# Performance work log

Measured on AMD Instinct MI355X. Metric: run time of the kernel, lower is better.

## Reference

```python
import jax, jax.numpy as jnp
import numpy as np

NUM_HEAD = 16

def _make_rope(max_len, dim_head, theta=10000.0):
    inv_freq = 1.0 / (theta ** (np.arange(0, dim_head, 2, dtype=np.float32) / dim_head))
    t = np.arange(max_len, dtype=np.float32)
    freqs = np.outer(t, inv_freq)  # [S, dim_head/2]
    return jnp.asarray(np.cos(freqs)), jnp.asarray(np.sin(freqs))

def setup_inputs() -> dict:
    key = jax.random.key(0)
    k1, k2, k3 = jax.random.split(key, 3)
    B, S, D = 2, 2048, 1024
    num_layer = 12
    std = 0.02 / np.sqrt(2 * num_layer)
    x = jax.random.normal(k1, (B, S, D), dtype=jnp.float32)
    wQKV = jax.random.normal(k2, (3 * D, D), dtype=jnp.float32) * std
    wOut = jax.random.normal(k3, (D, D), dtype=jnp.float32) * 0.02
    cos, sin = _make_rope(S, D // NUM_HEAD)
    return {"x": x, "wQKV": wQKV, "wOut": wOut, "cos": cos, "sin": sin}

def _apply_rope(t, cos, sin):
    # t: [B, H, S, dh]; cos/sin: [S, dh/2] -> broadcast [1,1,S,dh/2]
    te, to = t[..., ::2], t[..., 1::2]
    re = te * cos - to * sin
    ro = to * cos + te * sin
    return jnp.stack([re, ro], axis=-1).reshape(t.shape)

def reference(x, wQKV, wOut, cos, sin):
    B, S, D = x.shape
    H = NUM_HEAD
    dh = D // H
    qkv = x @ wQKV.T  # [B, S, 3D]
    q, k, v = jnp.split(qkv, 3, axis=-1)
    q = q.reshape(B, S, H, dh).transpose(0, 2, 1, 3)  # [B,H,S,dh]
    k = k.reshape(B, S, H, dh).transpose(0, 2, 1, 3)
    v = v.reshape(B, S, H, dh).transpose(0, 2, 1, 3)
    c = cos[:S][None, None]
    s = sin[:S][None, None]
    q = _apply_rope(q, c, s)
    k = _apply_rope(k, c, s)
    scores = jnp.einsum('bhsd,bhtd->bhst', q, k) / jnp.sqrt(jnp.asarray(dh, x.dtype))
    causal = jnp.tril(jnp.ones((S, S), dtype=bool))
    scores = jnp.where(causal, scores, jnp.asarray(-jnp.inf, scores.dtype))
    w = jax.nn.softmax(scores, axis=-1)
    out = jnp.einsum('bhst,bhtd->bhsd', w, v)  # [B,H,S,dh]
    out = out.transpose(0, 2, 1, 3).reshape(B, S, D)
    return out @ wOut.T
```

## Files before the change

kernel.cpp:

```cpp
#include <hip/hip_runtime.h>
#include <hip/hip_bf16.h>

typedef __attribute__((ext_vector_type(8))) short bf16x8;
typedef __attribute__((ext_vector_type(4))) short s16x4;
typedef __attribute__((ext_vector_type(4))) float f32x4;

__device__ __forceinline__ short f2bf(float f) {
    unsigned int u = __builtin_bit_cast(unsigned int, f);
    u += 0x7fffu + ((u >> 16) & 1u);
    return (short)(u >> 16);
}

#define GLDS(g, l) __builtin_amdgcn_global_load_lds( \
    (__attribute__((address_space(1))) void*)(g),    \
    (__attribute__((address_space(3))) void*)(l), 16, 0, 0)

#define BARSB() { __builtin_amdgcn_s_barrier(); __builtin_amdgcn_sched_barrier(0); }
#define VMC8()  { asm volatile("s_waitcnt vmcnt(8)" ::: "memory"); __builtin_amdgcn_sched_barrier(0); }
#define VMC7()  { asm volatile("s_waitcnt vmcnt(7)" ::: "memory"); __builtin_amdgcn_sched_barrier(0); }
#define VMC0()  { asm volatile("s_waitcnt vmcnt(0)" ::: "memory"); __builtin_amdgcn_sched_barrier(0); }

__global__ __launch_bounds__(256) void cvt_kernel(const float* __restrict__ in,
                                                  short* __restrict__ out, int n4) {
    int i = blockIdx.x * 256 + threadIdx.x;
    if (i >= n4) return;
    float4 v = reinterpret_cast<const float4*>(in)[i];
    s16x4 r = { f2bf(v.x), f2bf(v.y), f2bf(v.z), f2bf(v.w) };
    reinterpret_cast<s16x4*>(out)[i] = r;
}

#define LDP 72

__device__ __forceinline__ void load_a(const short* __restrict__ A, int wr, int lo, int hi,
                                       int mh, bf16x8 aF[4][2]) {
#pragma unroll
    for (int mi = 0; mi < 4; ++mi)
#pragma unroll
        for (int kk = 0; kk < 2; ++kk)
            aF[mi][kk] = *reinterpret_cast<const bf16x8*>(
                &A[(wr * 128 + mh * 64 + mi * 16 + lo) * 64 + (((kk * 4 + hi) ^ (lo & 7)) << 3)]);
}
__device__ __forceinline__ void load_b3(const short* __restrict__ B, int wc, int lo, int hi,
                                        bf16x8 bF[3][2]) {
#pragma unroll
    for (int ni = 0; ni < 3; ++ni)
#pragma unroll
        for (int kk = 0; kk < 2; ++kk)
            bF[ni][kk] = *reinterpret_cast<const bf16x8*>(
                &B[(wc * 48 + ni * 16 + lo) * 64 + (((kk * 4 + hi) ^ (lo & 7)) << 3)]);
}
__device__ __forceinline__ void mfma24(const bf16x8 aF[4][2], const bf16x8 bF[3][2],
                                       f32x4 acc[8][3], int mh) {
#pragma unroll
    for (int mi = 0; mi < 4; ++mi)
#pragma unroll
        for (int ni = 0; ni < 3; ++ni)
#pragma unroll
            for (int kk = 0; kk < 2; ++kk)
                acc[mh * 4 + mi][ni] = __builtin_amdgcn_mfma_f32_16x16x32_bf16(
                    aF[mi][kk], bF[ni][kk], acc[mh * 4 + mi][ni], 0, 0, 0);
}

__global__ __launch_bounds__(512, 1) void gemm_qkv_rope(
    const short* __restrict__ X, const short* __restrict__ W,
    const float* __restrict__ cosT, const float* __restrict__ sinT,
    short* __restrict__ Qo, short* __restrict__ Ko, short* __restrict__ Vo) {
    __shared__ short ldsA[2][16384];
    __shared__ short ldsB[2][12288];
    const int tid = threadIdx.x;
    const int lane = tid & 63;
    const int w = tid >> 6;
    const int lo = lane & 15, hi = lane >> 4;
    const int wr = w >> 2, wc = w & 3;
    const int lin = blockIdx.x;
    const int xcd = lin & 7;
    const int i_ = lin >> 3;
    const int m0 = ((xcd >> 1) * 4 + (i_ & 3)) * 256;
    const int n0 = ((xcd & 1) * 8 + (i_ >> 2)) * 192;

    f32x4 acc[8][3];
#pragma unroll
    for (int i = 0; i < 8; i++)
#pragma unroll
        for (int j = 0; j < 3; j++) acc[i][j] = {0.f, 0.f, 0.f, 0.f};

    const int srow8 = w * 8 + (lane >> 3);
    const int scx = (((lane & 7) ^ ((lane >> 3) & 7)) << 3);

#define STAGE_A(BUF, KT, IT) GLDS(X + (size_t)(m0 + (IT) * 64 + srow8) * 1024 + ((KT) << 6) + scx, \
                                  (char*)&ldsA[BUF][0] + (IT) * 8192 + w * 1024)
#define STAGE_B(BUF, KT, IT) GLDS(W + (size_t)(n0 + (IT) * 64 + srow8) * 1024 + ((KT) << 6) + scx, \
                                  (char*)&ldsB[BUF][0] + (IT) * 8192 + w * 1024)

    bf16x8 aF[4][2], bF[3][2];

    STAGE_B(0, 0, 0); STAGE_B(0, 0, 1); STAGE_B(0, 0, 2);
    STAGE_A(0, 0, 0); STAGE_A(0, 0, 1); STAGE_A(0, 0, 2); STAGE_A(0, 0, 3);

    for (int t = 0; t < 16; ++t) {
        const int c = t & 1;
        if (t < 15) {
            const int nb_ = c ^ 1, t1 = t + 1;
            STAGE_B(nb_, t1, 0); STAGE_B(nb_, t1, 1); STAGE_B(nb_, t1, 2);
            STAGE_A(nb_, t1, 0); STAGE_A(nb_, t1, 1); STAGE_A(nb_, t1, 2); STAGE_A(nb_, t1, 3);
            VMC7();
        } else {
            VMC0();
        }
        BARSB();
        load_a(&ldsA[c][0], wr, lo, hi, 0, aF);
        load_b3(&ldsB[c][0], wc, lo, hi, bF);
        mfma24(aF, bF, acc, 0);
        load_a(&ldsA[c][0], wr, lo, hi, 1, aF);
        mfma24(aF, bF, acc, 1);
        if (t < 15) BARSB();
    }
#undef STAGE_A
#undef STAGE_B

#pragma unroll
    for (int mi = 0; mi < 8; mi++) {
#pragma unroll
        for (int r = 0; r < 4; r++) {
            const int m = m0 + wr * 128 + mi * 16 + (hi << 2) + r;
            const int b_ = m >> 11;
            const int s_ = m & 2047;
#pragma unroll
            for (int ni = 0; ni < 3; ni++) {
                float v = acc[mi][ni][r];
                const int n = n0 + wc * 48 + ni * 16 + lo;
                const int region = n >> 10;
                const int c = n & 1023;
                const int h = c >> 6;
                const int d = c & 63;
                const size_t oidx = ((size_t)(b_ * 16 + h) * 2048 + s_) * 64 + d;
                if (region == 2) {
                    Vo[oidx] = f2bf(v);
                } else {
                    float other = __shfl_xor(v, 1, 64);
                    const int i2 = d >> 1;
                    float cs = cosT[s_ * 32 + i2];
                    float sn = sinT[s_ * 32 + i2];
                    float outv = (d & 1) ? (v * cs + other * sn) : (v * cs - other * sn);
                    if (region == 0) {
                        Qo[oidx] = f2bf(outv * 0.18033688f);
                    } else {
                        Ko[oidx] = f2bf(outv);
                    }
                }
            }
        }
    }
}

__device__ __forceinline__ void attn_tile_compute(
    const bf16x8 q0, const bf16x8 q1,
    const short* __restrict__ Ks,
    const short (*Vts)[LDP], short* __restrict__ Pw,
    const int lane, const int w, const bool diag,
    float& m_r, float& l_r, f32x4* __restrict__ o_acc) {
    const int lo = lane & 15, hi = lane >> 4;
    const int sx = lo & 7;

    f32x4 sc[4];
#pragma unroll
    for (int nb = 0; nb < 4; nb++) sc[nb] = {0.f, 0.f, 0.f, 0.f};
#pragma unroll
    for (int nb = 0; nb < 4; nb++) {
        const short* kr = &Ks[(nb * 16 + lo) * 64];
        bf16x8 k0 = *reinterpret_cast<const bf16x8*>(&kr[(hi ^ sx) << 3]);
        sc[nb] = __builtin_amdgcn_mfma_f32_16x16x32_bf16(k0, q0, sc[nb], 0, 0, 0);
        bf16x8 k1 = *reinterpret_cast<const bf16x8*>(&kr[((4 + hi) ^ sx) << 3]);
        sc[nb] = __builtin_amdgcn_mfma_f32_16x16x32_bf16(k1, q1, sc[nb], 0, 0, 0);
    }
    if (diag) {
        const int q_ = w * 16 + lo;
        const int kb = (hi << 2);
#pragma unroll
        for (int nb = 0; nb < 4; nb++) {
            const int k_ = nb * 16 + kb;
#pragma unroll
            for (int r = 0; r < 4; r++)
                if (k_ + r > q_) sc[nb][r] = -1e30f;
        }
    }

    float mx = sc[0][0];
#pragma unroll
    for (int nb = 0; nb < 4; nb++)
#pragma unroll
        for (int r = 0; r < 4; r++) mx = fmaxf(mx, sc[nb][r]);
    mx = fmaxf(mx, __shfl_xor(mx, 16, 64));
    mx = fmaxf(mx, __shfl_xor(mx, 32, 64));

    if (!__all(mx <= m_r + 8.0f)) {
        const float mnew = fmaxf(m_r, mx);
        const float alpha = __builtin_amdgcn_exp2f(m_r - mnew);
        m_r = mnew;
        l_r *= alpha;
        float aq[4];
#pragma unroll
        for (int r = 0; r < 4; r++) aq[r] = __shfl(alpha, (hi << 2) + r, 64);
#pragma unroll
        for (int db = 0; db < 4; db++)
#pragma unroll
            for (int r = 0; r < 4; r++) o_acc[db][r] *= aq[r];
    }

    float rs = 0.f;
#pragma unroll
    for (int nb = 0; nb < 4; nb++)
#pragma unroll
        for (int r = 0; r < 4; r++) {
            float e = __builtin_amdgcn_exp2f(sc[nb][r] - m_r);
            sc[nb][r] = e;
            rs += e;
        }
    rs += __shfl_xor(rs, 16, 64);
    rs += __shfl_xor(rs, 32, 64);
    l_r += rs;

    unsigned int* Pw32 = reinterpret_cast<unsigned int*>(Pw);
#pragma unroll
    for (int nb = 0; nb < 4; nb++)
#pragma unroll
        for (int rr = 0; rr < 2; rr++) {
            unsigned int pk;
            asm("v_cvt_pk_bf16_f32 %0, %1, %2"
                : "=v"(pk) : "v"(sc[nb][2 * rr]), "v"(sc[nb][2 * rr + 1]));
            Pw32[lo * (LDP / 2) + nb * 8 + (hi << 1) + rr] = pk;
        }

#pragma unroll
    for (int kk = 0; kk < 2; kk++) {
        bf16x8 pa = *reinterpret_cast<const bf16x8*>(&Pw[lo * LDP + kk * 32 + hi * 8]);
#pragma unroll
        for (int db = 0; db < 4; db++) {
            const int d = db * 16 + lo;
            const int tsw = (kk * 32 + hi * 8) ^ ((((d >> 3) & 7)) << 3);
            bf16x8 vb = *reinterpret_cast<const bf16x8*>(&Vts[d][tsw]);
            o_acc[db] = __builtin_amdgcn_mfma_f32_16x16x32_bf16(pa, vb, o_acc[db], 0, 0, 0);
        }
    }
}

__global__ __launch_bounds__(256) void attn_kernel(
    const short* __restrict__ Q, const short* __restrict__ K,
    const short* __restrict__ V, short* __restrict__ O) {
    __shared__ short Ks[2][64 * 64];
    __shared__ short Vts[2][64][LDP];
    __shared__ short Ps[4][16 * LDP];

    const int tid = threadIdx.x;
    const int lane = tid & 63;
    const int w = tid >> 6;
    const int lo = lane & 15, hi = lane >> 4;
    const int sx = lo & 7;
    const int lin = blockIdx.x;
    const int bh = lin & 31;
    const int qt = 31 - (lin >> 5);
    const int b_ = bh >> 4, h = bh & 15;
    const size_t base = (size_t)bh * 2048 * 64;

    const int krow = tid >> 2;
    const int cq = (tid & 3) * 2;
    const int ksw = krow & 7;

    bf16x8 q0, q1;
    {
        const short* src = Q + base + (size_t)(qt * 64 + krow) * 64 + cq * 8;
        bf16x8 a = *reinterpret_cast<const bf16x8*>(src);
        bf16x8 b = *reinterpret_cast<const bf16x8*>(src + 8);
        *reinterpret_cast<bf16x8*>(&Ks[0][krow * 64 + ((cq ^ ksw) << 3)]) = a;
        *reinterpret_cast<bf16x8*>(&Ks[0][krow * 64 + (((cq + 1) ^ ksw) << 3)]) = b;
        __syncthreads();
        q0 = *reinterpret_cast<const bf16x8*>(&Ks[0][(w * 16 + lo) * 64 + ((hi ^ sx) << 3)]);
        q1 = *reinterpret_cast<const bf16x8*>(&Ks[0][(w * 16 + lo) * 64 + (((4 + hi) ^ sx) << 3)]);
        __syncthreads();
    }

    float m_r = -1e30f, l_r = 0.f;
    f32x4 o_acc[4];
#pragma unroll
    for (int db = 0; db < 4; db++) o_acc[db] = {0.f, 0.f, 0.f, 0.f};

    const int u2 = tid >> 3;
    const int vdb8 = (tid & 7) * 8;
    const int vswz = (tid & 7) << 3;
    const int tw = (2 * u2) ^ vswz;

    bf16x8 kr0, kr1, vr0, vr1;
    kr0 = *reinterpret_cast<const bf16x8*>(K + base + (size_t)krow * 64 + cq * 8);
    kr1 = *reinterpret_cast<const bf16x8*>(K + base + (size_t)krow * 64 + cq * 8 + 8);
    vr0 = *reinterpret_cast<const bf16x8*>(V + base + (size_t)(2 * u2) * 64 + vdb8);
    vr1 = *reinterpret_cast<const bf16x8*>(V + base + (size_t)(2 * u2 + 1) * 64 + vdb8);

    int c = 0;
    for (int j = 0; j <= qt; j++) {
        *reinterpret_cast<bf16x8*>(&Ks[c][krow * 64 + ((cq ^ ksw) << 3)]) = kr0;
        *reinterpret_cast<bf16x8*>(&Ks[c][krow * 64 + (((cq + 1) ^ ksw) << 3)]) = kr1;
#pragma unroll
        for (int i = 0; i < 8; i++) {
            unsigned int pv = (unsigned int)(unsigned short)vr0[i] |
                              ((unsigned int)(unsigned short)vr1[i] << 16);
            *reinterpret_cast<unsigned int*>(&Vts[c][vdb8 + i][tw]) = pv;
        }
        __syncthreads();
        if (j < qt) {
            const size_t jb2 = (size_t)(j + 1) * 64;
            kr0 = *reinterpret_cast<const bf16x8*>(K + base + (jb2 + krow) * 64 + cq * 8);
            kr1 = *reinterpret_cast<const bf16x8*>(K + base + (jb2 + krow) * 64 + cq * 8 + 8);
            vr0 = *reinterpret_cast<const bf16x8*>(V + base + (jb2 + 2 * u2) * 64 + vdb8);
            vr1 = *reinterpret_cast<const bf16x8*>(V + base + (jb2 + 2 * u2 + 1) * 64 + vdb8);
        }

        attn_tile_compute(q0, q1, Ks[c], Vts[c], &Ps[w][0], lane, w, j == qt, m_r, l_r, o_acc);
        c ^= 1;
    }

    float inv[4];
#pragma unroll
    for (int r = 0; r < 4; r++) inv[r] = 1.f / __shfl(l_r, (hi << 2) + r, 64);

    short* Op = O + ((size_t)b_ * 2048) * 1024 + (size_t)h * 64;
#pragma unroll
    for (int r = 0; r < 4; r++) {
        const int row = qt * 64 + w * 16 + (hi << 2) + r;
#pragma unroll
        for (int db = 0; db < 4; db++)
            Op[(size_t)row * 1024 + db * 16 + lo] = f2bf(o_acc[db][r] * inv[r]);
    }
}

__global__ __launch_bounds__(256) void gemm_out(
    const short* __restrict__ A, const short* __restrict__ W,
    float* __restrict__ C) {
    __shared__ short As[2][128 * 64];
    __shared__ short Bs[2][128 * 64];
    const int tid = threadIdx.x;
    const int lane = tid & 63;
    const int w = tid >> 6;
    const int lo = lane & 15, hi = lane >> 4;
    const int wr = w >> 1, wc = w & 1;
    const int lin = blockIdx.x;
    const int wg = (lin & 7) * 32 + (lin >> 3);
    const int n0 = (wg & 7) * 128;
    const int m0 = (wg >> 3) * 128;
    const int K = 1024;

    f32x4 acc[4][4];
#pragma unroll
    for (int i = 0; i < 4; i++)
#pragma unroll
        for (int j = 0; j < 4; j++) acc[i][j] = {0.f, 0.f, 0.f, 0.f};

    const int srow = w * 8 + (lane >> 3);
    const int sc8 = (lane & 7) * 8;
    const short* gA = A + (size_t)(m0 + srow) * K + sc8;
    const short* gB = W + (size_t)(n0 + srow) * K + sc8;

#pragma unroll
    for (int it = 0; it < 4; it++)
        GLDS(gA + (size_t)it * 32 * K, (char*)As[0] + it * 4096 + w * 1024);
#pragma unroll
    for (int it = 0; it < 4; it++)
        GLDS(gB + (size_t)it * 32 * K, (char*)Bs[0] + it * 4096 + w * 1024);

    for (int t = 0; t < 16; t++) {
        const int c = t & 1;
        if (t < 15) {
            const int k1 = (t + 1) * 64;
#pragma unroll
            for (int it = 0; it < 4; it++)
                GLDS(gA + k1 + (size_t)it * 32 * K, (char*)As[c ^ 1] + it * 4096 + w * 1024);
#pragma unroll
            for (int it = 0; it < 4; it++)
                GLDS(gB + k1 + (size_t)it * 32 * K, (char*)Bs[c ^ 1] + it * 4096 + w * 1024);
            VMC8();
        } else {
            VMC0();
        }
        BARSB();
#pragma unroll
        for (int kk = 0; kk < 2; kk++) {
            bf16x8 a[4], b[4];
#pragma unroll
            for (int mi = 0; mi < 4; mi++)
                a[mi] = *reinterpret_cast<const bf16x8*>(
                    &As[c][(wr * 64 + mi * 16 + lo) * 64 + kk * 32 + hi * 8]);
#pragma unroll
            for (int ni = 0; ni < 4; ni++)
                b[ni] = *reinterpret_cast<const bf16x8*>(
                    &Bs[c][(wc * 64 + ni * 16 + lo) * 64 + kk * 32 + hi * 8]);
#pragma unroll
            for (int mi = 0; mi < 4; mi++)
#pragma unroll
                for (int ni = 0; ni < 4; ni++)
                    acc[mi][ni] = __builtin_amdgcn_mfma_f32_16x16x32_bf16(
                        a[mi], b[ni], acc[mi][ni], 0, 0, 0);
        }
        if (t < 15) BARSB();
    }

#pragma unroll
    for (int mi = 0; mi < 4; mi++) {
#pragma unroll
        for (int r = 0; r < 4; r++) {
            const int m = m0 + wr * 64 + mi * 16 + (hi << 2) + r;
#pragma unroll
            for (int ni = 0; ni < 4; ni++) {
                const int n = n0 + wc * 64 + ni * 16 + lo;
                C[(size_t)m * 1024 + n] = acc[mi][ni][r];
            }
        }
    }
}

extern "C" void kernel_launch(void* const* d_in, const int* in_sizes, int n_in,
                              void* d_out, int out_size, void* d_ws, size_t ws_size,
                              hipStream_t stream) {
    const float* x = (const float*)d_in[0];
    const float* wQKV = (const float*)d_in[1];
    const float* wOut = (const float*)d_in[2];
    const float* cosT = (const float*)d_in[3];
    const float* sinT = (const float*)d_in[4];
    float* out = (float*)d_out;

    char* ws = (char*)d_ws;
    const size_t MB = 1024 * 1024;
    short* xb    = (short*)(ws);
    short* wqkvb = (short*)(ws + 8 * MB);
    short* woutb = (short*)(ws + 14 * MB);
    short* Qbuf  = (short*)(ws + 16 * MB);
    short* Kbuf  = (short*)(ws + 24 * MB);
    short* Vbuf  = (short*)(ws + 32 * MB);
    short* Obuf  = (short*)(ws + 40 * MB);

    cvt_kernel<<<4096, 256, 0, stream>>>(x, xb, 1048576);
    cvt_kernel<<<3072, 256, 0, stream>>>(wQKV, wqkvb, 786432);
    cvt_kernel<<<1024, 256, 0, stream>>>(wOut, woutb, 262144);

    gemm_qkv_rope<<<256, 512, 0, stream>>>(xb, wqkvb, cosT, sinT, Qbuf, Kbuf, Vbuf);
    attn_kernel<<<1024, 256, 0, stream>>>(Qbuf, Kbuf, Vbuf, Obuf);
    gemm_out<<<256, 256, 0, stream>>>(Obuf, woutb, out);
}
```

Baseline: 124.2 us.

## Retile QKV GEMM to 128x128 blocks and fuse fp32-to-bf16 conversion launches

The three fp32-to-bf16 conversion launches become one kernel that picks its source buffer from the block index, saving two launch overheads. The QKV+RoPE GEMM moves from 256x192 tiles with 512 threads (256 blocks) to 128x128 tiles with 256 threads (768 blocks), with a 4x4 MFMA accumulator per wave and a Q/K/V region that is uniform per block. The aim is better occupancy and load balance across CUs, at the cost of less operand reuse per tile. The new LDS layout also drops the XOR swizzle, so the fragment reads may hit LDS bank conflicts.

```diff
diff --git a/kernel.cpp b/kernel.cpp
--- a/kernel.cpp
+++ b/kernel.cpp
@@ -17,13 +17,19 @@
 
 #define BARSB() { __builtin_amdgcn_s_barrier(); __builtin_amdgcn_sched_barrier(0); }
 #define VMC8()  { asm volatile("s_waitcnt vmcnt(8)" ::: "memory"); __builtin_amdgcn_sched_barrier(0); }
-#define VMC7()  { asm volatile("s_waitcnt vmcnt(7)" ::: "memory"); __builtin_amdgcn_sched_barrier(0); }
 #define VMC0()  { asm volatile("s_waitcnt vmcnt(0)" ::: "memory"); __builtin_amdgcn_sched_barrier(0); }
 
-__global__ __launch_bounds__(256) void cvt_kernel(const float* __restrict__ in,
-                                                  short* __restrict__ out, int n4) {
-    int i = blockIdx.x * 256 + threadIdx.x;
-    if (i >= n4) return;
+__global__ __launch_bounds__(256) void cvt_fused(const float* __restrict__ x,
+                                                 const float* __restrict__ wq,
+                                                 const float* __restrict__ wo,
+                                                 short* __restrict__ xb,
+                                                 short* __restrict__ wqb,
+                                                 short* __restrict__ wob) {
+    const int b = blockIdx.x;
+    const float* in; short* out; int i;
+    if (b < 4096)      { in = x;  out = xb;  i = b * 256 + threadIdx.x; }
+    else if (b < 7168) { in = wq; out = wqb; i = (b - 4096) * 256 + threadIdx.x; }
+    else               { in = wo; out = wob; i = (b - 7168) * 256 + threadIdx.x; }
     float4 v = reinterpret_cast<const float4*>(in)[i];
     s16x4 r = { f2bf(v.x), f2bf(v.y), f2bf(v.z), f2bf(v.w) };
     reinterpret_cast<s16x4*>(out)[i] = r;
@@ -31,105 +37,90 @@
 
 #define LDP 72
 
-__device__ __forceinline__ void load_a(const short* __restrict__ A, int wr, int lo, int hi,
-                                       int mh, bf16x8 aF[4][2]) {
-#pragma unroll
-    for (int mi = 0; mi < 4; ++mi)
-#pragma unroll
-        for (int kk = 0; kk < 2; ++kk)
-            aF[mi][kk] = *reinterpret_cast<const bf16x8*>(
-                &A[(wr * 128 + mh * 64 + mi * 16 + lo) * 64 + (((kk * 4 + hi) ^ (lo & 7)) << 3)]);
-}
-__device__ __forceinline__ void load_b3(const short* __restrict__ B, int wc, int lo, int hi,
-                                        bf16x8 bF[3][2]) {
-#pragma unroll
-    for (int ni = 0; ni < 3; ++ni)
-#pragma unroll
-        for (int kk = 0; kk < 2; ++kk)
-            bF[ni][kk] = *reinterpret_cast<const bf16x8*>(
-                &B[(wc * 48 + ni * 16 + lo) * 64 + (((kk * 4 + hi) ^ (lo & 7)) << 3)]);
-}
-__device__ __forceinline__ void mfma24(const bf16x8 aF[4][2], const bf16x8 bF[3][2],
-                                       f32x4 acc[8][3], int mh) {
-#pragma unroll
-    for (int mi = 0; mi < 4; ++mi)
-#pragma unroll
-        for (int ni = 0; ni < 3; ++ni)
-#pragma unroll
-            for (int kk = 0; kk < 2; ++kk)
-                acc[mh * 4 + mi][ni] = __builtin_amdgcn_mfma_f32_16x16x32_bf16(
-                    aF[mi][kk], bF[ni][kk], acc[mh * 4 + mi][ni], 0, 0, 0);
-}
-
-__global__ __launch_bounds__(512, 1) void gemm_qkv_rope(
+__global__ __launch_bounds__(256) void gemm_qkv_rope(
     const short* __restrict__ X, const short* __restrict__ W,
     const float* __restrict__ cosT, const float* __restrict__ sinT,
     short* __restrict__ Qo, short* __restrict__ Ko, short* __restrict__ Vo) {
-    __shared__ short ldsA[2][16384];
-    __shared__ short ldsB[2][12288];
+    __shared__ short As[2][128 * 64];
+    __shared__ short Bs[2][128 * 64];
     const int tid = threadIdx.x;
     const int lane = tid & 63;
     const int w = tid >> 6;
     const int lo = lane & 15, hi = lane >> 4;
-    const int wr = w >> 2, wc = w & 3;
+    const int wr = w >> 1, wc = w & 1;
     const int lin = blockIdx.x;
     const int xcd = lin & 7;
     const int i_ = lin >> 3;
-    const int m0 = ((xcd >> 1) * 4 + (i_ & 3)) * 256;
-    const int n0 = ((xcd & 1) * 8 + (i_ >> 2)) * 192;
-
-    f32x4 acc[8][3];
-#pragma unroll
-    for (int i = 0; i < 8; i++)
-#pragma unroll
-        for (int j = 0; j < 3; j++) acc[i][j] = {0.f, 0.f, 0.f, 0.f};
-
-    const int srow8 = w * 8 + (lane >> 3);
-    const int scx = (((lane & 7) ^ ((lane >> 3) & 7)) << 3);
-
-#define STAGE_A(BUF, KT, IT) GLDS(X + (size_t)(m0 + (IT) * 64 + srow8) * 1024 + ((KT) << 6) + scx, \
-                                  (char*)&ldsA[BUF][0] + (IT) * 8192 + w * 1024)
-#define STAGE_B(BUF, KT, IT) GLDS(W + (size_t)(n0 + (IT) * 64 + srow8) * 1024 + ((KT) << 6) + scx, \
-                                  (char*)&ldsB[BUF][0] + (IT) * 8192 + w * 1024)
-
-    bf16x8 aF[4][2], bF[3][2];
-
-    STAGE_B(0, 0, 0); STAGE_B(0, 0, 1); STAGE_B(0, 0, 2);
-    STAGE_A(0, 0, 0); STAGE_A(0, 0, 1); STAGE_A(0, 0, 2); STAGE_A(0, 0, 3);
-
-    for (int t = 0; t < 16; ++t) {
+    const int m0 = ((xcd >> 1) * 8 + (i_ & 7)) * 128;
+    const int n0 = ((xcd & 1) * 12 + (i_ >> 3)) * 128;
+    const int K = 1024;
+
+    f32x4 acc[4][4];
+#pragma unroll
+    for (int i = 0; i < 4; i++)
+#pragma unroll
+        for (int j = 0; j < 4; j++) acc[i][j] = {0.f, 0.f, 0.f, 0.f};
+
+    const int srow = w * 8 + (lane >> 3);
+    const int sc8 = (lane & 7) * 8;
+    const short* gA = X + (size_t)(m0 + srow) * K + sc8;
+    const short* gB = W + (size_t)(n0 + srow) * K + sc8;
+
+#pragma unroll
+    for (int it = 0; it < 4; it++)
+        GLDS(gA + (size_t)it * 32 * K, (char*)As[0] + it * 4096 + w * 1024);
+#pragma unroll
+    for (int it = 0; it < 4; it++)
+        GLDS(gB + (size_t)it * 32 * K, (char*)Bs[0] + it * 4096 + w * 1024);
+
+    for (int t = 0; t < 16; t++) {
         const int c = t & 1;
         if (t < 15) {
-            const int nb_ = c ^ 1, t1 = t + 1;
-            STAGE_B(nb_, t1, 0); STAGE_B(nb_, t1, 1); STAGE_B(nb_, t1, 2);
-            STAGE_A(nb_, t1, 0); STAGE_A(nb_, t1, 1); STAGE_A(nb_, t1, 2); STAGE_A(nb_, t1, 3);
-            VMC7();
+            const int k1 = (t + 1) * 64;
+#pragma unroll
+            for (int it = 0; it < 4; it++)
+                GLDS(gA + k1 + (size_t)it * 32 * K, (char*)As[c ^ 1] + it * 4096 + w * 1024);
+#pragma unroll
+            for (int it = 0; it < 4; it++)
+                GLDS(gB + k1 + (size_t)it * 32 * K, (char*)Bs[c ^ 1] + it * 4096 + w * 1024);
+            VMC8();
         } else {
             VMC0();
         }
         BARSB();
-        load_a(&ldsA[c][0], wr, lo, hi, 0, aF);
-        load_b3(&ldsB[c][0], wc, lo, hi, bF);
-        mfma24(aF, bF, acc, 0);
-        load_a(&ldsA[c][0], wr, lo, hi, 1, aF);
-        mfma24(aF, bF, acc, 1);
+#pragma unroll
+        for (int kk = 0; kk < 2; kk++) {
+            bf16x8 a[4], b[4];
+#pragma unroll
+            for (int mi = 0; mi < 4; mi++)
+                a[mi] = *reinterpret_cast<const bf16x8*>(
+                    &As[c][(wr * 64 + mi * 16 + lo) * 64 + kk * 32 + hi * 8]);
+#pragma unroll
+            for (int ni = 0; ni < 4; ni++)
+                b[ni] = *reinterpret_cast<const bf16x8*>(
+                    &Bs[c][(wc * 64 + ni * 16 + lo) * 64 + kk * 32 + hi * 8]);
+#pragma unroll
+            for (int mi = 0; mi < 4; mi++)
+#pragma unroll
+                for (int ni = 0; ni < 4; ni++)
+                    acc[mi][ni] = __builtin_amdgcn_mfma_f32_16x16x32_bf16(
+                        a[mi], b[ni], acc[mi][ni], 0, 0, 0);
+        }
         if (t < 15) BARSB();
     }
-#undef STAGE_A
-#undef STAGE_B
-
-#pragma unroll
-    for (int mi = 0; mi < 8; mi++) {
+
+    const int region = n0 >> 10;
+#pragma unroll
+    for (int mi = 0; mi < 4; mi++) {
 #pragma unroll
         for (int r = 0; r < 4; r++) {
-            const int m = m0 + wr * 128 + mi * 16 + (hi << 2) + r;
+            const int m = m0 + wr * 64 + mi * 16 + (hi << 2) + r;
             const int b_ = m >> 11;
             const int s_ = m & 2047;
 #pragma unroll
-            for (int ni = 0; ni < 3; ni++) {
+            for (int ni = 0; ni < 4; ni++) {
                 float v = acc[mi][ni][r];
-                const int n = n0 + wc * 48 + ni * 16 + lo;
-                const int region = n >> 10;
+                const int n = n0 + wc * 64 + ni * 16 + lo;
                 const int c = n & 1023;
                 const int h = c >> 6;
                 const int d = c & 63;
@@ -436,11 +427,8 @@
     short* Vbuf  = (short*)(ws + 32 * MB);
     short* Obuf  = (short*)(ws + 40 * MB);
 
-    cvt_kernel<<<4096, 256, 0, stream>>>(x, xb, 1048576);
-    cvt_kernel<<<3072, 256, 0, stream>>>(wQKV, wqkvb, 786432);
-    cvt_kernel<<<1024, 256, 0, stream>>>(wOut, woutb, 262144);
-
-    gemm_qkv_rope<<<256, 512, 0, stream>>>(xb, wqkvb, cosT, sinT, Qbuf, Kbuf, Vbuf);
+    cvt_fused<<<8192, 256, 0, stream>>>(x, wQKV, wOut, xb, wqkvb, woutb);
+    gemm_qkv_rope<<<768, 256, 0, stream>>>(xb, wqkvb, cosT, sinT, Qbuf, Kbuf, Vbuf);
     attn_kernel<<<1024, 256, 0, stream>>>(Qbuf, Kbuf, Vbuf, Obuf);
     gemm_out<<<256, 256, 0, stream>>>(Obuf, woutb, out);
 }
```

Result: slower. 145.8 us (+17.4%).
